# Kernel optimization log

Hardware: AMD Instinct MI355X
Metric: run time of the kernel (lower is better)

## Reference

```python
import jax, jax.numpy as jnp
import numpy as np

D, NH, DH, NL, NP, NLAYERS, DFF = 256, 8, 32, 3, 4, 6, 1024
SHAPES = ((64, 64), (32, 32), (16, 16))  # (H, W) per level, strides 8/16/32 of a 512px image


def layer_norm(x, g, b):
    m = jnp.mean(x, -1, keepdims=True)
    v = jnp.mean((x - m) ** 2, -1, keepdims=True)
    return (x - m) * jax.lax.rsqrt(v + 1e-5) * g + b


def _ref_points():
    pts = []
    for (h, w) in SHAPES:
        ry = (jnp.arange(h, dtype=jnp.float32) + 0.5) / h
        rx = (jnp.arange(w, dtype=jnp.float32) + 0.5) / w
        yy, xx = jnp.meshgrid(ry, rx, indexing='ij')
        pts.append(jnp.stack([xx.reshape(-1), yy.reshape(-1)], -1))
    return jnp.concatenate(pts, 0)  # [Q, 2] (x, y) normalized; valid_ratios == 1


def _sample_level(value_l, loc, h, w):
    # value_l: [B, NH, h*w, DH]; loc: [B, Q, NH, NP, 2] normalized in [0,1]
    # grid_sample(align_corners=False, padding zeros): pixel = loc*size - 0.5
    B, Q = loc.shape[0], loc.shape[1]
    x = loc[..., 0] * w - 0.5
    y = loc[..., 1] * h - 0.5
    x0f = jnp.floor(x); y0f = jnp.floor(y)
    lx = x - x0f; ly = y - y0f
    x0 = x0f.astype(jnp.int32); y0 = y0f.astype(jnp.int32)
    out = jnp.zeros((B, NH, Q, NP, DH), value_l.dtype)
    corners = ((0, 0, (1 - lx) * (1 - ly)), (1, 0, lx * (1 - ly)),
               (0, 1, (1 - lx) * ly), (1, 1, lx * ly))
    for dx, dy, wgt in corners:
        xi = x0 + dx; yi = y0 + dy
        valid = ((xi >= 0) & (xi < w) & (yi >= 0) & (yi < h)).astype(value_l.dtype)
        idx = jnp.clip(yi, 0, h - 1) * w + jnp.clip(xi, 0, w - 1)        # [B,Q,NH,NP]
        idx_f = jnp.transpose(idx, (0, 2, 1, 3)).reshape(B, NH, Q * NP)
        v = jnp.take_along_axis(value_l, idx_f[..., None], axis=2)       # [B,NH,Q*NP,DH]
        v = v.reshape(B, NH, Q, NP, DH)
        w_f = jnp.transpose(wgt * valid, (0, 2, 1, 3))                   # [B,NH,Q,NP]
        out = out + v * w_f[..., None]
    return out


def setup_inputs():
    key = jax.random.key(0)
    ks = iter(jax.random.split(key, 64))
    d = {}
    B = 4
    for i, (h, w) in enumerate(SHAPES):
        d[f'src{i}'] = jax.random.normal(next(ks), (B, D, h, w), jnp.float32)
        d[f'pos{i}'] = jax.random.normal(next(ks), (B, D, h, w), jnp.float32) * 0.1
    s = 0.02
    p = lambda shape: jax.random.normal(next(ks), shape, jnp.float32) * s
    d['level_embed'] = p((NL, D))
    d['W_off'] = p((NLAYERS, D, NH * NL * NP * 2)); d['b_off'] = p((NLAYERS, NH * NL * NP * 2))
    d['W_attn'] = p((NLAYERS, D, NH * NL * NP));   d['b_attn'] = p((NLAYERS, NH * NL * NP))
    d['W_val'] = p((NLAYERS, D, D)); d['b_val'] = p((NLAYERS, D))
    d['W_out'] = p((NLAYERS, D, D)); d['b_out'] = p((NLAYERS, D))
    d['ln1_g'] = jnp.ones((NLAYERS, D)); d['ln1_b'] = jnp.zeros((NLAYERS, D))
    d['W_ff1'] = p((NLAYERS, D, DFF)); d['b_ff1'] = p((NLAYERS, DFF))
    d['W_ff2'] = p((NLAYERS, DFF, D)); d['b_ff2'] = p((NLAYERS, D))
    d['ln2_g'] = jnp.ones((NLAYERS, D)); d['ln2_b'] = jnp.zeros((NLAYERS, D))
    return d


def reference(src0, src1, src2, pos0, pos1, pos2, level_embed,
              W_off, b_off, W_attn, b_attn, W_val, b_val, W_out, b_out,
              ln1_g, ln1_b, W_ff1, b_ff1, W_ff2, b_ff2, ln2_g, ln2_b):
    srcs = (src0, src1, src2)
    poss = (pos0, pos1, pos2)
    B = src0.shape[0]
    # flatten levels: [B, C, H, W] -> [B, H*W, C]; add per-level embedding to pos
    src = jnp.concatenate([s.reshape(B, D, -1).transpose(0, 2, 1) for s in srcs], 1)
    pos = jnp.concatenate([poss[l].reshape(B, D, -1).transpose(0, 2, 1) + level_embed[l]
                           for l in range(NL)], 1)
    Q = src.shape[1]
    ref = _ref_points()  # [Q, 2]
    x = src
    for i in range(NLAYERS):
        q = x + pos
        off = (q @ W_off[i] + b_off[i]).reshape(B, Q, NH, NL, NP, 2)
        aw = jax.nn.softmax((q @ W_attn[i] + b_attn[i]).reshape(B, Q, NH, NL * NP), -1)
        aw = aw.reshape(B, Q, NH, NL, NP)
        val = (x @ W_val[i] + b_val[i]).reshape(B, Q, NH, DH)
        attn_out = jnp.zeros((B, Q, NH, DH), x.dtype)
        start = 0
        for l, (h, w) in enumerate(SHAPES):
            hw = h * w
            v_l = jnp.transpose(val[:, start:start + hw], (0, 2, 1, 3))  # [B,NH,hw,DH]
            wh = jnp.array([w, h], jnp.float32)
            loc = ref[None, :, None, None, :] + off[:, :, :, l] / wh     # [B,Q,NH,NP,2]
            smp = _sample_level(v_l, loc, h, w)                          # [B,NH,Q,NP,DH]
            attn_out = attn_out + jnp.einsum('bhqpd,bqhp->bqhd', smp, aw[:, :, :, l])
            start += hw
        attn_out = attn_out.reshape(B, Q, D) @ W_out[i] + b_out[i]
        x = layer_norm(x + attn_out, ln1_g[i], ln1_b[i])
        ff = jax.nn.relu(x @ W_ff1[i] + b_ff1[i]) @ W_ff2[i] + b_ff2[i]
        x = layer_norm(x + ff, ln2_g[i], ln2_b[i])
    return x  # memory: [B, Q, D]
```

## Files before the change

### kernel.cpp

```cpp
#include <hip/hip_runtime.h>


#define DMODEL 256
#define NLAYERS 6
#define BATCH 4
#define QTOT 5376
#define MROWS (BATCH * QTOT)

typedef __bf16 bf16x8 __attribute__((ext_vector_type(8)));
typedef __bf16 bf16x4 __attribute__((ext_vector_type(4)));
typedef float floatx4 __attribute__((ext_vector_type(4)));

#define GLOAD(gp, lp)                                                          \
  __builtin_amdgcn_global_load_lds(                                            \
      (__attribute__((address_space(1))) void*)(gp),                           \
      (__attribute__((address_space(3))) void*)(lp), 16, 0, 0)

__global__ __launch_bounds__(256) void flatten_kernel(
    const float* __restrict__ s0, const float* __restrict__ p0,
    const float* __restrict__ s1, const float* __restrict__ p1,
    const float* __restrict__ s2, const float* __restrict__ p2,
    const float* __restrict__ lvl, __bf16* __restrict__ xb,
    __bf16* __restrict__ posb, __bf16* __restrict__ qb) {
  __shared__ float ls[32][33];
  __shared__ float lp[32][33];
  int b = blockIdx.y;
  int tile = blockIdx.x;
  const float* sp; const float* pp; int l, hw, tp, td, qbase;
  if (tile < 1024)      { l = 0; hw = 4096; int t = tile;        td = t & 7; tp = t >> 3; qbase = 0; sp = s0; pp = p0; }
  else if (tile < 1280) { l = 1; hw = 1024; int t = tile - 1024; td = t & 7; tp = t >> 3; qbase = 4096; sp = s1; pp = p1; }
  else                  { l = 2; hw = 256;  int t = tile - 1280; td = t & 7; tp = t >> 3; qbase = 5120; sp = s2; pp = p2; }
  int tx = threadIdx.x & 31, ty = threadIdx.x >> 5;
  int d0 = td * 32, pbase = tp * 32;
#pragma unroll
  for (int r = 0; r < 4; ++r) {
    int dl = r * 8 + ty;
    size_t gi = ((size_t)(b * DMODEL + d0 + dl)) * hw + pbase + tx;
    ls[dl][tx] = sp[gi];
    lp[dl][tx] = pp[gi];
  }
  __syncthreads();
  int d = d0 + tx;
  float lv = lvl[l * DMODEL + d];
#pragma unroll
  for (int r = 0; r < 4; ++r) {
    int pl = r * 8 + ty;
    size_t bq = (size_t)b * QTOT + qbase + pbase + pl;
    float xv = ls[tx][pl];
    float pv = lp[tx][pl] + lv;
    xb[bq * DMODEL + d]   = (__bf16)xv;
    posb[bq * DMODEL + d] = (__bf16)pv;
    qb[bq * DMODEL + d]   = (__bf16)(xv + pv);
  }
}

__global__ __launch_bounds__(256) void pack3_kernel(
    const float* __restrict__ Wout, const float* __restrict__ Wff1,
    const float* __restrict__ Wff2, __bf16* __restrict__ wout_t,
    __bf16* __restrict__ wff1_t, __bf16* __restrict__ wff2_t) {
  __shared__ float ls[32][33];
  int l = blockIdx.y;
  int tt = blockIdx.x;
  const float* src; __bf16* dst; int K, N, u, tilesx;
  if (tt < 64)       { src = Wout + (size_t)l * 256 * 256;  dst = wout_t + (size_t)l * 256 * 256;  K = 256;  N = 256;  u = tt;        tilesx = 8;  }
  else if (tt < 320) { src = Wff1 + (size_t)l * 256 * 1024; dst = wff1_t + (size_t)l * 1024 * 256; K = 256;  N = 1024; u = tt - 64;  tilesx = 32; }
  else               { src = Wff2 + (size_t)l * 1024 * 256; dst = wff2_t + (size_t)l * 256 * 1024; K = 1024; N = 256;  u = tt - 320; tilesx = 8;  }
  int n0 = (u % tilesx) * 32, k0 = (u / tilesx) * 32;
  int tx = threadIdx.x & 31, ty = threadIdx.x >> 5;
#pragma unroll
  for (int r = 0; r < 4; ++r)
    ls[ty + r * 8][tx] = src[(size_t)(k0 + ty + r * 8) * N + n0 + tx];
  __syncthreads();
#pragma unroll
  for (int r = 0; r < 4; ++r)
    dst[(size_t)(n0 + ty + r * 8) * K + k0 + tx] = (__bf16)ls[tx][ty + r * 8];
}

__global__ __launch_bounds__(256) void pack_qv_t_kernel(
    const float* __restrict__ Woff, const float* __restrict__ Wattn,
    const float* __restrict__ Wval, __bf16* __restrict__ Wt) {
  __shared__ float ls[32][33];
  int l = blockIdx.z;
  int tc = blockIdx.x, k0 = blockIdx.y * 32;
  int tx = threadIdx.x & 31, ty = threadIdx.x >> 5;
  const float* src; int n0, sn;
  if (tc < 6)       { src = Woff  + (size_t)l * 256 * 192; n0 = tc * 32;        sn = 192; }
  else if (tc < 9)  { src = Wattn + (size_t)l * 256 * 96;  n0 = (tc - 6) * 32;  sn = 96;  }
  else if (tc < 12) { src = nullptr; n0 = 0; sn = 0; }
  else              { src = Wval  + (size_t)l * 256 * 256; n0 = (tc - 12) * 32; sn = 256; }
#pragma unroll
  for (int r = 0; r < 4; ++r)
    ls[ty + r * 8][tx] = src ? src[(size_t)(k0 + ty + r * 8) * sn + n0 + tx] : 0.f;
  __syncthreads();
  __bf16* dst = Wt + (size_t)l * 640 * 256 + (size_t)tc * 32 * 256;
#pragma unroll
  for (int r = 0; r < 4; ++r)
    dst[(size_t)(ty + r * 8) * 256 + k0 + tx] = (__bf16)ls[tx][ty + r * 8];
}

__global__ __launch_bounds__(640) void pack_bias_kernel(
    const float* __restrict__ boff, const float* __restrict__ battn,
    const float* __restrict__ bval, float* __restrict__ bc) {
  int l = blockIdx.x, n = threadIdx.x;
  float b = 0.f;
  if (n < 192)       b = boff[l * 192 + n];
  else if (n < 288)  b = battn[l * 96 + (n - 192)];
  else if (n >= 384) b = bval[l * 256 + (n - 384)];
  bc[l * 640 + n] = b;
}

#define GEMM_CORE(A_, B_, K_)                                                  \
  for (int k0 = 0; k0 < (K_); k0 += 32) {                                      \
    __syncthreads();                                                           \
    _Pragma("unroll")                                                          \
    for (int cc = 0; cc < 2; ++cc) {                                           \
      int c = wid * 2 + cc;                                                    \
      GLOAD((A_) + (size_t)c * 16 * (K_) + k0, As + c * 512);                  \
      GLOAD((B_) + (size_t)c * 16 * (K_) + k0, Bs + c * 512);                  \
    }                                                                          \
    __syncthreads();                                                           \
    bf16x8 af[4], bfr[4];                                                      \
    _Pragma("unroll")                                                          \
    for (int i = 0; i < 4; ++i)                                                \
      af[i] = *(const bf16x8*)&As[(wr * 64 + i * 16 + (lane & 15)) * 32 + (lane >> 4) * 8]; \
    _Pragma("unroll")                                                          \
    for (int j = 0; j < 4; ++j)                                                \
      bfr[j] = *(const bf16x8*)&Bs[(wc * 64 + j * 16 + (lane & 15)) * 32 + (lane >> 4) * 8]; \
    _Pragma("unroll")                                                          \
    for (int i = 0; i < 4; ++i)                                                \
      _Pragma("unroll")                                                        \
      for (int j = 0; j < 4; ++j)                                              \
        acc[i][j] = __builtin_amdgcn_mfma_f32_16x16x32_bf16(af[i], bfr[j], acc[i][j], 0, 0, 0); \
  }

template<int RELU, int BF16OUT>
__global__ __launch_bounds__(256) void gemm_bf16_kernel(
    const __bf16* __restrict__ A, const __bf16* __restrict__ Wt,
    const float* __restrict__ bias, float* __restrict__ C,
    __bf16* __restrict__ Cb, int N, int K) {
  __shared__ __bf16 As[128 * 32];
  __shared__ __bf16 Bs[128 * 32];
  int t = threadIdx.x;
  int lane = t & 63, wid = t >> 6;
  int wr = wid >> 1, wc = wid & 1;
  int row0 = blockIdx.y * 128;
  int n0 = blockIdx.x * 128;
  floatx4 acc[4][4] = {};
  int srow = lane >> 2;
  int skoff = (lane & 3) * 8;
  const __bf16* Abase = A + (size_t)(row0 + srow) * K + skoff;
  const __bf16* Bbase = Wt + (size_t)(n0 + srow) * K + skoff;
  GEMM_CORE(Abase, Bbase, K)
  int orow = row0 + wr * 64 + (lane >> 4) * 4;
  int ocol = n0 + wc * 64 + (lane & 15);
#pragma unroll
  for (int i = 0; i < 4; ++i)
#pragma unroll
    for (int j = 0; j < 4; ++j) {
      int col = ocol + j * 16;
      float bv = bias[col];
#pragma unroll
      for (int r = 0; r < 4; ++r) {
        int row = orow + i * 16 + r;
        float v = acc[i][j][r] + bv;
        if (RELU) v = fmaxf(v, 0.f);
        if (BF16OUT) Cb[(size_t)row * N + col] = (__bf16)v;
        else         C[(size_t)row * N + col] = v;
      }
    }
}

template<int RELU>
__global__ __launch_bounds__(256) void gemm64_bf16_kernel(
    const __bf16* __restrict__ A, const __bf16* __restrict__ Wt,
    const float* __restrict__ bias, __bf16* __restrict__ Cb, int N, int K) {
  __shared__ __bf16 As[64 * 32];
  __shared__ __bf16 Bs[128 * 32];
  int t = threadIdx.x;
  int lane = t & 63, wid = t >> 6;
  int wr = wid >> 1, wc = wid & 1;
  int row0 = blockIdx.y * 64;
  int n0 = blockIdx.x * 128;
  floatx4 acc[2][4] = {};
  int srow = lane >> 2;
  int skoff = (lane & 3) * 8;
  const __bf16* Abase = A + (size_t)(row0 + srow) * K + skoff;
  const __bf16* Bbase = Wt + (size_t)(n0 + srow) * K + skoff;
  for (int k0 = 0; k0 < K; k0 += 32) {
    __syncthreads();
#pragma unroll
    for (int cc = 0; cc < 3; ++cc) {
      int c = wid * 3 + cc;
      if (c < 4) GLOAD(Abase + (size_t)c * 16 * K + k0, As + c * 512);
      else       GLOAD(Bbase + (size_t)(c - 4) * 16 * K + k0, Bs + (c - 4) * 512);
    }
    __syncthreads();
    bf16x8 af[2], bfr[4];
#pragma unroll
    for (int i = 0; i < 2; ++i)
      af[i] = *(const bf16x8*)&As[(wr * 32 + i * 16 + (lane & 15)) * 32 + (lane >> 4) * 8];
#pragma unroll
    for (int j = 0; j < 4; ++j)
      bfr[j] = *(const bf16x8*)&Bs[(wc * 64 + j * 16 + (lane & 15)) * 32 + (lane >> 4) * 8];
#pragma unroll
    for (int i = 0; i < 2; ++i)
#pragma unroll
      for (int j = 0; j < 4; ++j)
        acc[i][j] = __builtin_amdgcn_mfma_f32_16x16x32_bf16(af[i], bfr[j], acc[i][j], 0, 0, 0);
  }
  int orow = row0 + wr * 32 + (lane >> 4) * 4;
  int ocol = n0 + wc * 64 + (lane & 15);
#pragma unroll
  for (int i = 0; i < 2; ++i)
#pragma unroll
    for (int j = 0; j < 4; ++j) {
      int col = ocol + j * 16;
      float bv = bias[col];
#pragma unroll
      for (int r = 0; r < 4; ++r) {
        int row = orow + i * 16 + r;
        float v = acc[i][j][r] + bv;
        if (RELU) v = fmaxf(v, 0.f);
        Cb[(size_t)row * N + col] = (__bf16)v;
      }
    }
}

__global__ __launch_bounds__(256) void gemm_qv_kernel(
    const __bf16* __restrict__ qb, const __bf16* __restrict__ xb,
    const __bf16* __restrict__ Wt, const float* __restrict__ bias,
    float* __restrict__ qproj, __bf16* __restrict__ valb) {
  __shared__ __bf16 As[128 * 32];
  __shared__ __bf16 Bs[128 * 32];
  int t = threadIdx.x;
  int lane = t & 63, wid = t >> 6;
  int wr = wid >> 1, wc = wid & 1;
  int bn = blockIdx.x;
  int row0 = blockIdx.y * 128;
  int n0 = bn * 128;
  const __bf16* A = (bn < 3) ? qb : xb;
  floatx4 acc[4][4] = {};
  int srow = lane >> 2;
  int skoff = (lane & 3) * 8;
  const __bf16* Abase = A + (size_t)(row0 + srow) * 256 + skoff;
  const __bf16* Bbase = Wt + (size_t)(n0 + srow) * 256 + skoff;
  GEMM_CORE(Abase, Bbase, 256)
  int orow = row0 + wr * 64 + (lane >> 4) * 4;
  int ocol = wc * 64 + (lane & 15);
#pragma unroll
  for (int i = 0; i < 4; ++i)
#pragma unroll
    for (int j = 0; j < 4; ++j) {
      int col = ocol + j * 16;
      float bv = bias[n0 + col];
#pragma unroll
      for (int r = 0; r < 4; ++r) {
        int row = orow + i * 16 + r;
        float v = acc[i][j][r] + bv;
        if (bn < 3) qproj[(size_t)row * 384 + n0 + col] = v;
        else        valb[(size_t)row * 256 + (n0 - 384) + col] = (__bf16)v;
      }
    }
}

__global__ __launch_bounds__(256) void deform_kernel(
    const __bf16* __restrict__ val, const float* __restrict__ qproj,
    __bf16* __restrict__ out) {
  int bid = blockIdx.x;
  int b = bid / 672, r = bid % 672;
  int j = threadIdx.x >> 5;
  int jx = j & 3, jy = j >> 2;
  int wsrc, qbase, px, py;
  if (r < 512)      { wsrc = 64; qbase = 0;    int ty = r >> 4, tx = r & 15;          px = tx * 4 + jx; py = ty * 2 + jy; }
  else if (r < 640) { wsrc = 32; qbase = 4096; int t = r - 512; int ty = t >> 3, tx = t & 7; px = tx * 4 + jx; py = ty * 2 + jy; }
  else              { wsrc = 16; qbase = 5120; int t = r - 640; int ty = t >> 2, tx = t & 3; px = tx * 4 + jx; py = ty * 2 + jy; }
  int q = qbase + py * wsrc + px;
  int bq = b * QTOT + q;
  int tq = threadIdx.x & 31;
  int hid = tq >> 2, dq = (tq & 3) * 8;

  float inv = 1.0f / (float)wsrc;
  float refx = ((float)px + 0.5f) * inv;
  float refy = ((float)py + 0.5f) * inv;

  const float* base = qproj + (size_t)bq * 384;
  float aw[12], ob[24];
  *(float4*)&aw[0] = *(const float4*)(base + 192 + hid * 12);
  *(float4*)&aw[4] = *(const float4*)(base + 192 + hid * 12 + 4);
  *(float4*)&aw[8] = *(const float4*)(base + 192 + hid * 12 + 8);
#pragma unroll
  for (int i = 0; i < 6; ++i)
    *(float4*)&ob[i * 4] = *(const float4*)(base + hid * 24 + i * 4);

  float mx = -1e30f;
#pragma unroll
  for (int k = 0; k < 12; ++k) mx = fmaxf(mx, aw[k]);
  float s = 0.f;
#pragma unroll
  for (int k = 0; k < 12; ++k) { aw[k] = __expf(aw[k] - mx); s += aw[k]; }
  float invs = 1.0f / s;
#pragma unroll
  for (int k = 0; k < 12; ++k) aw[k] *= invs;

  const __bf16* vb = val + ((size_t)b * QTOT) * DMODEL + hid * 32 + dq;

  const int starts[3] = {0, 4096, 5120};
  const int wls[3] = {64, 32, 16};
  float acc[8] = {};
#pragma unroll
  for (int l = 0; l < 3; ++l) {
    int wl = wls[l];
    float fwl = (float)wl;
    const __bf16* vlb = vb + (size_t)starts[l] * DMODEL;
#pragma unroll
    for (int pp = 0; pp < 4; ++pp) {
      float awp = aw[l * 4 + pp];
      float fx = refx * fwl + ob[(l * 4 + pp) * 2 + 0] - 0.5f;
      float fy = refy * fwl + ob[(l * 4 + pp) * 2 + 1] - 0.5f;
      float x0f = floorf(fx), y0f = floorf(fy);
      float lx = fx - x0f, ly = fy - y0f;
      int x0 = (int)x0f, y0 = (int)y0f;
      float wx0 = ((unsigned)x0 < (unsigned)wl) ? (1.f - lx) : 0.f;
      float wx1 = ((unsigned)(x0 + 1) < (unsigned)wl) ? lx : 0.f;
      float wy0 = (((unsigned)y0 < (unsigned)wl) ? (1.f - ly) : 0.f) * awp;
      float wy1 = (((unsigned)(y0 + 1) < (unsigned)wl) ? ly : 0.f) * awp;
      int xc0 = min(max(x0, 0), wl - 1);
      int xc1 = min(max(x0 + 1, 0), wl - 1);
      int yc0 = min(max(y0, 0), wl - 1);
      int yc1 = min(max(y0 + 1, 0), wl - 1);
      const __bf16* r0 = vlb + (size_t)(yc0 * wl) * DMODEL;
      const __bf16* r1 = vlb + (size_t)(yc1 * wl) * DMODEL;
      bf16x8 v00 = *(const bf16x8*)(r0 + (size_t)xc0 * DMODEL);
      bf16x8 v01 = *(const bf16x8*)(r0 + (size_t)xc1 * DMODEL);
      bf16x8 v10 = *(const bf16x8*)(r1 + (size_t)xc0 * DMODEL);
      bf16x8 v11 = *(const bf16x8*)(r1 + (size_t)xc1 * DMODEL);
      float w00 = wx0 * wy0, w01 = wx1 * wy0;
      float w10 = wx0 * wy1, w11 = wx1 * wy1;
#pragma unroll
      for (int e = 0; e < 8; ++e) {
        float v = w00 * (float)v00[e] + w01 * (float)v01[e] +
                  w10 * (float)v10[e] + w11 * (float)v11[e];
        acc[e] += v;
      }
    }
  }
  bf16x8 o;
#pragma unroll
  for (int e = 0; e < 8; ++e) o[e] = (__bf16)acc[e];
  *(bf16x8*)(out + (size_t)bq * DMODEL + hid * 32 + dq) = o;
}

template<int QB>
__global__ __launch_bounds__(256) void add_ln_kernel(
    const __bf16* __restrict__ xin, const __bf16* __restrict__ res,
    const float* __restrict__ g, const float* __restrict__ bta,
    __bf16* __restrict__ xout, const __bf16* __restrict__ posb,
    __bf16* __restrict__ qb, float* __restrict__ fout) {
  int row = blockIdx.x * 4 + (threadIdx.x >> 6);
  int lane = threadIdx.x & 63;
  int c = lane * 4;
  bf16x4 xv4 = *(const bf16x4*)(xin + (size_t)row * DMODEL + c);
  bf16x4 rv4 = *(const bf16x4*)(res + (size_t)row * DMODEL + c);
  float xv0 = (float)xv4[0] + (float)rv4[0];
  float xv1 = (float)xv4[1] + (float)rv4[1];
  float xv2 = (float)xv4[2] + (float)rv4[2];
  float xv3 = (float)xv4[3] + (float)rv4[3];
  float s = xv0 + xv1 + xv2 + xv3;
  float sq = xv0 * xv0 + xv1 * xv1 + xv2 * xv2 + xv3 * xv3;
#pragma unroll
  for (int o = 32; o >= 1; o >>= 1) {
    s += __shfl_xor(s, o);
    sq += __shfl_xor(sq, o);
  }
  float mean = s * (1.f / 256.f);
  float var = sq * (1.f / 256.f) - mean * mean;
  float rstd = rsqrtf(var + 1e-5f);
  float4 gv = *(const float4*)(g + c);
  float4 bv = *(const float4*)(bta + c);
  float o0 = (xv0 - mean) * rstd * gv.x + bv.x;
  float o1 = (xv1 - mean) * rstd * gv.y + bv.y;
  float o2 = (xv2 - mean) * rstd * gv.z + bv.z;
  float o3 = (xv3 - mean) * rstd * gv.w + bv.w;
  bf16x4 ob;
  ob[0] = (__bf16)o0; ob[1] = (__bf16)o1;
  ob[2] = (__bf16)o2; ob[3] = (__bf16)o3;
  *(bf16x4*)(xout + (size_t)row * DMODEL + c) = ob;
  if (QB) {
    bf16x4 pv = *(const bf16x4*)(posb + (size_t)row * DMODEL + c);
    bf16x4 qv;
    qv[0] = (__bf16)(o0 + (float)pv[0]); qv[1] = (__bf16)(o1 + (float)pv[1]);
    qv[2] = (__bf16)(o2 + (float)pv[2]); qv[3] = (__bf16)(o3 + (float)pv[3]);
    *(bf16x4*)(qb + (size_t)row * DMODEL + c) = qv;
  }
  if (fout) {
    float4 f4 = make_float4(o0, o1, o2, o3);
    *(float4*)(fout + (size_t)row * DMODEL + c) = f4;
  }
}

extern "C" void kernel_launch(void* const* d_in, const int* in_sizes, int n_in,
                              void* d_out, int out_size, void* d_ws, size_t ws_size,
                              hipStream_t stream) {
  const float* src0 = (const float*)d_in[0];
  const float* pos0 = (const float*)d_in[1];
  const float* src1 = (const float*)d_in[2];
  const float* pos1 = (const float*)d_in[3];
  const float* src2 = (const float*)d_in[4];
  const float* pos2 = (const float*)d_in[5];
  const float* lvl  = (const float*)d_in[6];
  const float* W_off  = (const float*)d_in[7];
  const float* b_off  = (const float*)d_in[8];
  const float* W_attn = (const float*)d_in[9];
  const float* b_attn = (const float*)d_in[10];
  const float* W_val  = (const float*)d_in[11];
  const float* b_val  = (const float*)d_in[12];
  const float* W_out  = (const float*)d_in[13];
  const float* b_out  = (const float*)d_in[14];
  const float* ln1g = (const float*)d_in[15];
  const float* ln1b = (const float*)d_in[16];
  const float* W_ff1 = (const float*)d_in[17];
  const float* b_ff1 = (const float*)d_in[18];
  const float* W_ff2 = (const float*)d_in[19];
  const float* b_ff2 = (const float*)d_in[20];
  const float* ln2g = (const float*)d_in[21];
  const float* ln2b = (const float*)d_in[22];

  const size_t M = (size_t)MROWS;
  char* w = (char*)d_ws;
  __bf16* xb    = (__bf16*)w;                w += M * 256 * 2;
  __bf16* posb  = (__bf16*)w;                w += M * 256 * 2;
  __bf16* qb    = (__bf16*)w;                w += M * 256 * 2;
  float*  qproj = (float*)w;                 w += M * 384 * 4;
  __bf16* valb  = (__bf16*)w;                w += M * 256 * 2;
  __bf16* ffh   = (__bf16*)w;                w += M * 1024 * 2;
  __bf16* wqv_t = (__bf16*)w;                w += (size_t)NLAYERS * 640 * 256 * 2;
  __bf16* wout_t= (__bf16*)w;                w += (size_t)NLAYERS * 256 * 256 * 2;
  __bf16* wff1_t= (__bf16*)w;                w += (size_t)NLAYERS * 1024 * 256 * 2;
  __bf16* wff2_t= (__bf16*)w;                w += (size_t)NLAYERS * 256 * 1024 * 2;
  float*  bqv   = (float*)w;                 w += (size_t)NLAYERS * 640 * 4;
  __bf16* attn_bf = qb;
  __bf16* proj  = ffh;
  __bf16* ffres = (__bf16*)qproj;

  pack_qv_t_kernel<<<dim3(20, 8, NLAYERS), 256, 0, stream>>>(W_off, W_attn, W_val, wqv_t);
  pack_bias_kernel<<<NLAYERS, 640, 0, stream>>>(b_off, b_attn, b_val, bqv);
  pack3_kernel<<<dim3(576, NLAYERS), 256, 0, stream>>>(
      W_out, W_ff1, W_ff2, wout_t, wff1_t, wff2_t);

  flatten_kernel<<<dim3(1344, BATCH), 256, 0, stream>>>(
      src0, pos0, src1, pos1, src2, pos2, lvl, xb, posb, qb);

  const int MT = MROWS / 128;
  const int MT64 = MROWS / 64;
  for (int i = 0; i < NLAYERS; ++i) {
    gemm_qv_kernel<<<dim3(5, MT), 256, 0, stream>>>(
        qb, xb, wqv_t + (size_t)i * 640 * 256, bqv + i * 640, qproj, valb);
    deform_kernel<<<MROWS / 8, 256, 0, stream>>>(valb, qproj, attn_bf);
    gemm64_bf16_kernel<0><<<dim3(2, MT64), 256, 0, stream>>>(
        attn_bf, wout_t + (size_t)i * 256 * 256, b_out + i * 256, proj, 256, 256);
    add_ln_kernel<0><<<MROWS / 4, 256, 0, stream>>>(
        xb, proj, ln1g + i * 256, ln1b + i * 256, xb, nullptr, nullptr, nullptr);
    gemm_bf16_kernel<1, 1><<<dim3(8, MT), 256, 0, stream>>>(
        xb, wff1_t + (size_t)i * 1024 * 256, b_ff1 + i * 1024, nullptr, ffh, 1024, 256);
    gemm64_bf16_kernel<0><<<dim3(2, MT64), 256, 0, stream>>>(
        ffh, wff2_t + (size_t)i * 256 * 1024, b_ff2 + i * 256, ffres, 256, 1024);
    float* fout = (i == NLAYERS - 1) ? (float*)d_out : nullptr;
    add_ln_kernel<1><<<MROWS / 4, 256, 0, stream>>>(
        xb, ffres, ln2g + i * 256, ln2b + i * 256, xb, posb, qb, fout);
  }
}
```

Baseline: 829.9 us.

## Double-buffer LDS tiles in bf16 GEMM kernels to overlap loads with MFMA

The GEMM main loops now use two LDS buffers. The next K-slice is issued via global_load_lds while MFMAs run on the current slice, and there is a single barrier per iteration instead of two. This is meant to hide global-to-LDS latency behind compute. It doubles LDS usage per block, which may reduce occupancy. It also relies on the barrier to cover async load completion (vmcnt), so correctness depends on how the compiler inserts waits.

Result: no change. 844.3 us (+1.7%).

```diff
diff --git a/kernel.cpp b/kernel.cpp
--- a/kernel.cpp
+++ b/kernel.cpp
@@ -109,28 +109,45 @@
   bc[l * 640 + n] = b;
 }
 
-#define GEMM_CORE(A_, B_, K_)                                                  \
-  for (int k0 = 0; k0 < (K_); k0 += 32) {                                      \
-    __syncthreads();                                                           \
+#define GEMM_CORE_DB(A_, B_, K_)                                               \
+  {                                                                            \
+    int cur = 0;                                                               \
     _Pragma("unroll")                                                          \
     for (int cc = 0; cc < 2; ++cc) {                                           \
       int c = wid * 2 + cc;                                                    \
-      GLOAD((A_) + (size_t)c * 16 * (K_) + k0, As + c * 512);                  \
-      GLOAD((B_) + (size_t)c * 16 * (K_) + k0, Bs + c * 512);                  \
+      GLOAD((A_) + (size_t)c * 16 * (K_), As + c * 512);                       \
+      GLOAD((B_) + (size_t)c * 16 * (K_), Bs + c * 512);                       \
     }                                                                          \
     __syncthreads();                                                           \
-    bf16x8 af[4], bfr[4];                                                      \
-    _Pragma("unroll")                                                          \
-    for (int i = 0; i < 4; ++i)                                                \
-      af[i] = *(const bf16x8*)&As[(wr * 64 + i * 16 + (lane & 15)) * 32 + (lane >> 4) * 8]; \
-    _Pragma("unroll")                                                          \
-    for (int j = 0; j < 4; ++j)                                                \
-      bfr[j] = *(const bf16x8*)&Bs[(wc * 64 + j * 16 + (lane & 15)) * 32 + (lane >> 4) * 8]; \
-    _Pragma("unroll")                                                          \
-    for (int i = 0; i < 4; ++i)                                                \
-      _Pragma("unroll")                                                        \
-      for (int j = 0; j < 4; ++j)                                              \
-        acc[i][j] = __builtin_amdgcn_mfma_f32_16x16x32_bf16(af[i], bfr[j], acc[i][j], 0, 0, 0); \
+    for (int k0 = 0; k0 < (K_); k0 += 32) {                                    \
+      if (k0 + 32 < (K_)) {                                                    \
+        int nb = (cur ^ 1) * 4096;                                             \
+        _Pragma("unroll")                                                      \
+        for (int cc = 0; cc < 2; ++cc) {                                       \
+          int c = wid * 2 + cc;                                                \
+          GLOAD((A_) + (size_t)c * 16 * (K_) + k0 + 32, As + nb + c * 512);    \
+          GLOAD((B_) + (size_t)c * 16 * (K_) + k0 + 32, Bs + nb + c * 512);    \
+        }                                                                      \
+      }                                                                        \
+      {                                                                        \
+        const __bf16* Asb = As + cur * 4096;                                   \
+        const __bf16* Bsb = Bs + cur * 4096;                                   \
+        bf16x8 af[4], bfr[4];                                                  \
+        _Pragma("unroll")                                                      \
+        for (int i = 0; i < 4; ++i)                                            \
+          af[i] = *(const bf16x8*)&Asb[(wr * 64 + i * 16 + (lane & 15)) * 32 + (lane >> 4) * 8]; \
+        _Pragma("unroll")                                                      \
+        for (int j = 0; j < 4; ++j)                                            \
+          bfr[j] = *(const bf16x8*)&Bsb[(wc * 64 + j * 16 + (lane & 15)) * 32 + (lane >> 4) * 8]; \
+        _Pragma("unroll")                                                      \
+        for (int i = 0; i < 4; ++i)                                            \
+          _Pragma("unroll")                                                    \
+          for (int j = 0; j < 4; ++j)                                          \
+            acc[i][j] = __builtin_amdgcn_mfma_f32_16x16x32_bf16(af[i], bfr[j], acc[i][j], 0, 0, 0); \
+      }                                                                        \
+      __syncthreads();                                                         \
+      cur ^= 1;                                                                \
+    }                                                                          \
   }
 
 template<int RELU, int BF16OUT>
@@ -138,8 +155,8 @@
     const __bf16* __restrict__ A, const __bf16* __restrict__ Wt,
     const float* __restrict__ bias, float* __restrict__ C,
     __bf16* __restrict__ Cb, int N, int K) {
-  __shared__ __bf16 As[128 * 32];
-  __shared__ __bf16 Bs[128 * 32];
+  __shared__ __bf16 As[2 * 4096];
+  __shared__ __bf16 Bs[2 * 4096];
   int t = threadIdx.x;
   int lane = t & 63, wid = t >> 6;
   int wr = wid >> 1, wc = wid & 1;
@@ -150,7 +167,7 @@
   int skoff = (lane & 3) * 8;
   const __bf16* Abase = A + (size_t)(row0 + srow) * K + skoff;
   const __bf16* Bbase = Wt + (size_t)(n0 + srow) * K + skoff;
-  GEMM_CORE(Abase, Bbase, K)
+  GEMM_CORE_DB(Abase, Bbase, K)
   int orow = row0 + wr * 64 + (lane >> 4) * 4;
   int ocol = n0 + wc * 64 + (lane & 15);
 #pragma unroll
@@ -174,8 +191,8 @@
 __global__ __launch_bounds__(256) void gemm64_bf16_kernel(
     const __bf16* __restrict__ A, const __bf16* __restrict__ Wt,
     const float* __restrict__ bias, __bf16* __restrict__ Cb, int N, int K) {
-  __shared__ __bf16 As[64 * 32];
-  __shared__ __bf16 Bs[128 * 32];
+  __shared__ __bf16 As[2 * 2048];
+  __shared__ __bf16 Bs[2 * 4096];
   int t = threadIdx.x;
   int lane = t & 63, wid = t >> 6;
   int wr = wid >> 1, wc = wid & 1;
@@ -186,27 +203,44 @@
   int skoff = (lane & 3) * 8;
   const __bf16* Abase = A + (size_t)(row0 + srow) * K + skoff;
   const __bf16* Bbase = Wt + (size_t)(n0 + srow) * K + skoff;
-  for (int k0 = 0; k0 < K; k0 += 32) {
-    __syncthreads();
+  {
+    int cur = 0;
 #pragma unroll
     for (int cc = 0; cc < 3; ++cc) {
       int c = wid * 3 + cc;
-      if (c < 4) GLOAD(Abase + (size_t)c * 16 * K + k0, As + c * 512);
-      else       GLOAD(Bbase + (size_t)(c - 4) * 16 * K + k0, Bs + (c - 4) * 512);
+      if (c < 4) GLOAD(Abase + (size_t)c * 16 * K, As + c * 512);
+      else       GLOAD(Bbase + (size_t)(c - 4) * 16 * K, Bs + (c - 4) * 512);
     }
     __syncthreads();
-    bf16x8 af[2], bfr[4];
-#pragma unroll
-    for (int i = 0; i < 2; ++i)
-      af[i] = *(const bf16x8*)&As[(wr * 32 + i * 16 + (lane & 15)) * 32 + (lane >> 4) * 8];
-#pragma unroll
-    for (int j = 0; j < 4; ++j)
-      bfr[j] = *(const bf16x8*)&Bs[(wc * 64 + j * 16 + (lane & 15)) * 32 + (lane >> 4) * 8];
-#pragma unroll
-    for (int i = 0; i < 2; ++i)
-#pragma unroll
-      for (int j = 0; j < 4; ++j)
-        acc[i][j] = __builtin_amdgcn_mfma_f32_16x16x32_bf16(af[i], bfr[j], acc[i][j], 0, 0, 0);
+    for (int k0 = 0; k0 < K; k0 += 32) {
+      if (k0 + 32 < K) {
+        int nbA = (cur ^ 1) * 2048, nbB = (cur ^ 1) * 4096;
+#pragma unroll
+        for (int cc = 0; cc < 3; ++cc) {
+          int c = wid * 3 + cc;
+          if (c < 4) GLOAD(Abase + (size_t)c * 16 * K + k0 + 32, As + nbA + c * 512);
+          else       GLOAD(Bbase + (size_t)(c - 4) * 16 * K + k0 + 32, Bs + nbB + (c - 4) * 512);
+        }
+      }
+      {
+        const __bf16* Asb = As + cur * 2048;
+        const __bf16* Bsb = Bs + cur * 4096;
+        bf16x8 af[2], bfr[4];
+#pragma unroll
+        for (int i = 0; i < 2; ++i)
+          af[i] = *(const bf16x8*)&Asb[(wr * 32 + i * 16 + (lane & 15)) * 32 + (lane >> 4) * 8];
+#pragma unroll
+        for (int j = 0; j < 4; ++j)
+          bfr[j] = *(const bf16x8*)&Bsb[(wc * 64 + j * 16 + (lane & 15)) * 32 + (lane >> 4) * 8];
+#pragma unroll
+        for (int i = 0; i < 2; ++i)
+#pragma unroll
+          for (int j = 0; j < 4; ++j)
+            acc[i][j] = __builtin_amdgcn_mfma_f32_16x16x32_bf16(af[i], bfr[j], acc[i][j], 0, 0, 0);
+      }
+      __syncthreads();
+      cur ^= 1;
+    }
   }
   int orow = row0 + wr * 32 + (lane >> 4) * 4;
   int ocol = n0 + wc * 64 + (lane & 15);
@@ -230,8 +264,8 @@
     const __bf16* __restrict__ qb, const __bf16* __restrict__ xb,
     const __bf16* __restrict__ Wt, const float* __restrict__ bias,
     float* __restrict__ qproj, __bf16* __restrict__ valb) {
-  __shared__ __bf16 As[128 * 32];
-  __shared__ __bf16 Bs[128 * 32];
+  __shared__ __bf16 As[2 * 4096];
+  __shared__ __bf16 Bs[2 * 4096];
   int t = threadIdx.x;
   int lane = t & 63, wid = t >> 6;
   int wr = wid >> 1, wc = wid & 1;
@@ -244,7 +278,7 @@
   int skoff = (lane & 3) * 8;
   const __bf16* Abase = A + (size_t)(row0 + srow) * 256 + skoff;
   const __bf16* Bbase = Wt + (size_t)(n0 + srow) * 256 + skoff;
-  GEMM_CORE(Abase, Bbase, 256)
+  GEMM_CORE_DB(Abase, Bbase, 256)
   int orow = row0 + wr * 64 + (lane >> 4) * 4;
   int ocol = wc * 64 + (lane & 15);
 #pragma unroll
```
